# Kernel optimization log

Measured on AMD Instinct MI355X. Metric: run time of the kernel, lower is better.

Reference implementation:

```python
import jax, jax.numpy as jnp
import numpy as np

E = 1024      # embed_dim (== embed_dim_)
NH = 8        # num_heads
HD = E // NH  # head_dim
BS1 = 2048
BS2 = 2048
EPS = 1e-5


def _layernorm(x, g, b):
    m = jnp.mean(x, axis=-1, keepdims=True)
    v = jnp.mean(jnp.square(x - m), axis=-1, keepdims=True)
    return (x - m) * jax.lax.rsqrt(v + EPS) * g + b


def setup_inputs() -> dict:
    key = jax.random.key(0)
    ks = jax.random.split(key, 16)
    s = 1.0 / np.sqrt(E)
    s4 = 1.0 / np.sqrt(4 * E)
    inp = {
        "x1": jax.random.normal(ks[0], (BS1, E), jnp.float32),
        "x2": jax.random.normal(ks[1], (BS2, E), jnp.float32),
        "Wq": jax.random.uniform(ks[2], (E, E), jnp.float32, -s, s),
        "bq": jax.random.uniform(ks[3], (E,), jnp.float32, -s, s),
        "Wk": jax.random.uniform(ks[4], (E, E), jnp.float32, -s, s),
        "bk": jax.random.uniform(ks[5], (E,), jnp.float32, -s, s),
        "Wv": jax.random.uniform(ks[6], (E, E), jnp.float32, -s, s),
        "bv": jax.random.uniform(ks[7], (E,), jnp.float32, -s, s),
        "Wo": jax.random.uniform(ks[8], (E, E), jnp.float32, -s, s),
        "bo": jax.random.uniform(ks[9], (E,), jnp.float32, -s, s),
        "W1": jax.random.uniform(ks[10], (4 * E, E), jnp.float32, -s, s),
        "b1": jax.random.uniform(ks[11], (4 * E,), jnp.float32, -s, s),
        "W2": jax.random.uniform(ks[12], (E, 4 * E), jnp.float32, -s4, s4),
        "b2": jax.random.uniform(ks[13], (E,), jnp.float32, -s4, s4),
        "g1": jnp.ones((E,), jnp.float32),
        "be1": jnp.zeros((E,), jnp.float32),
        "g2": jnp.ones((E,), jnp.float32),
        "be2": jnp.zeros((E,), jnp.float32),
    }
    return inp


def reference(x1, x2, Wq, bq, Wk, bk, Wv, bv, Wo, bo, W1, b1, W2, b2, g1, be1, g2, be2):
    scale = HD ** -0.5
    # Projections; attention runs over the batch axis (n=bs1, m=bs2)
    q = (x1 @ Wq.T + bq).reshape(BS1, NH, HD)   # [n,h,d]
    k = (x2 @ Wk.T + bk).reshape(BS2, NH, HD)   # [m,h,d]
    v = (x2 @ Wv.T + bv).reshape(BS2, NH, HD)   # [m,h,d]
    scores = jnp.einsum('nhd,mhd->nmh', q, k) * scale  # [n,m,h]
    # NOTE: faithful to source: softmax over the HEADS axis (dim=-1)
    probs = jax.nn.softmax(scores, axis=-1)
    # dropout is identity in eval mode
    attn = jnp.einsum('nmh,mhd->nhd', probs, v).reshape(BS1, E)
    attn = attn @ Wo.T + bo
    h = _layernorm(x1 + attn, g1, be1)
    ffn = jax.nn.relu(h @ W1.T + b1) @ W2.T + b2
    return _layernorm(h + ffn, g2, be2)
```

## Files before the change

kernel.cpp:

```cpp
#include <hip/hip_runtime.h>

#define BS 2048
#define EMB 1024
#define NHEAD 8
#define HDIM 128

typedef unsigned short u16;
typedef __attribute__((ext_vector_type(8))) short bf16x8;
typedef __attribute__((ext_vector_type(4))) float f32x4;

__device__ __forceinline__ u16 f32_bf16(float f) {
  unsigned u = __float_as_uint(f);
  u += 0x7fffu + ((u >> 16) & 1u);
  return (u16)(u >> 16);
}
__device__ __forceinline__ float bf2f(u16 x) {
  return __uint_as_float((unsigned)x << 16);
}

__device__ __forceinline__ void gld_lds16(const void* g, void* l) {
  __builtin_amdgcn_global_load_lds(
      (const __attribute__((address_space(1))) void*)g,
      (__attribute__((address_space(3))) void*)l, 16, 0, 0);
}

struct CvtArgs { const float* src[8]; };
__global__ __launch_bounds__(256) void cvt_all(CvtArgs a, u16* __restrict__ dst) {
  long i = (long)blockIdx.x * 256 + threadIdx.x;
  int seg = (int)(i >> 18);
  const float* src; long b;
  if (seg < 2)       { src = a.src[0]; b = 0; }
  else if (seg < 4)  { src = a.src[1]; b = 2L << 18; }
  else if (seg == 4) { src = a.src[2]; b = 4L << 18; }
  else if (seg == 5) { src = a.src[3]; b = 5L << 18; }
  else if (seg == 6) { src = a.src[4]; b = 6L << 18; }
  else if (seg == 7) { src = a.src[5]; b = 7L << 18; }
  else if (seg < 12) { src = a.src[6]; b = 8L << 18; }
  else               { src = a.src[7]; b = 12L << 18; }
  float4 v = ((const float4*)src)[i - b];
  ushort4 o;
  o.x = f32_bf16(v.x); o.y = f32_bf16(v.y); o.z = f32_bf16(v.z); o.w = f32_bf16(v.w);
  ((ushort4*)dst)[i] = o;
}

__device__ __forceinline__ void gemm_core(
    const u16* __restrict__ A, const u16* __restrict__ B, void* __restrict__ Cp,
    const float* __restrict__ bias, int K, int lda, int ldb, int ldc,
    long cbase, int mode, int relu, int m0, int n0) {
  __shared__ __align__(16) u16 As[128 * 32];
  __shared__ __align__(16) u16 Bs[128 * 32];
  const int t = threadIdx.x;
  const int lane = t & 63, l15 = lane & 15, quad = lane >> 4;
  const int wv = t >> 6, wr = wv & 1, wc = wv >> 1;
  const int wbase = t & ~63;

  f32x4 acc[4][4];
#pragma unroll
  for (int r = 0; r < 4; ++r)
#pragma unroll
    for (int c = 0; c < 4; ++c) acc[r][c] = (f32x4){0.f, 0.f, 0.f, 0.f};

  for (int k0 = 0; k0 < K; k0 += 32) {
#pragma unroll
    for (int i = 0; i < 2; ++i) {
      int s = i * 256 + t;
      gld_lds16(A + (long)(m0 + (s >> 2)) * lda + k0 + (s & 3) * 8,
                As + (i * 256 + wbase) * 8);
    }
#pragma unroll
    for (int i = 0; i < 2; ++i) {
      int s = i * 256 + t;
      gld_lds16(B + (long)(n0 + (s >> 2)) * ldb + k0 + (s & 3) * 8,
                Bs + (i * 256 + wbase) * 8);
    }
    __syncthreads();
    bf16x8 fa[4], fb[4];
#pragma unroll
    for (int r = 0; r < 4; ++r)
      fa[r] = *(const bf16x8*)&As[(wr * 64 + r * 16 + l15) * 32 + quad * 8];
#pragma unroll
    for (int c = 0; c < 4; ++c)
      fb[c] = *(const bf16x8*)&Bs[(wc * 64 + c * 16 + l15) * 32 + quad * 8];
#pragma unroll
    for (int r = 0; r < 4; ++r)
#pragma unroll
      for (int c = 0; c < 4; ++c)
        acc[r][c] = __builtin_amdgcn_mfma_f32_16x16x32_bf16(fa[r], fb[c], acc[r][c], 0, 0, 0);
    __syncthreads();
  }

#pragma unroll
  for (int r = 0; r < 4; ++r)
#pragma unroll
    for (int c = 0; c < 4; ++c) {
      const int m = m0 + wr * 64 + r * 16 + quad * 4;
      const int n = n0 + wc * 64 + c * 16 + l15;
      const float bv = bias ? bias[n] : 0.f;
      f32x4 v = acc[r][c];
      if (mode == 2) {
        ushort4 o;
        o.x = f32_bf16(v[0] + bv);
        o.y = f32_bf16(v[1] + bv);
        o.z = f32_bf16(v[2] + bv);
        o.w = f32_bf16(v[3] + bv);
        *(ushort4*)((u16*)Cp + cbase + (long)n * ldc + m) = o;
      } else {
#pragma unroll
        for (int i = 0; i < 4; ++i) {
          float x = v[i] + bv;
          if (relu) x = fmaxf(x, 0.f);
          if (mode == 0)
            ((float*)Cp)[cbase + (long)(m + i) * ldc + n] = x;
          else
            ((u16*)Cp)[cbase + (long)(m + i) * ldc + n] = f32_bf16(x);
        }
      }
    }
}

__global__ __launch_bounds__(256) void gemm_bt_k(
    const u16* __restrict__ A, const u16* __restrict__ B, void* __restrict__ C,
    const float* __restrict__ bias, int K, int lda, int ldb, int ldc,
    long aOffZ, long bOffZ, long cOffZ, int mode, int relu) {
  gemm_core(A + (long)blockIdx.z * aOffZ, B + (long)blockIdx.z * bOffZ, C, bias,
            K, lda, ldb, ldc, (long)blockIdx.z * cOffZ, mode, relu,
            blockIdx.y * 128, blockIdx.x * 128);
}

__global__ __launch_bounds__(256) void qkv_kernel(
    const u16* __restrict__ x1b, const u16* __restrict__ x2b,
    const u16* __restrict__ Wqb, const u16* __restrict__ Wkb, const u16* __restrict__ Wvb,
    const float* __restrict__ bq, const float* __restrict__ bk, const float* __restrict__ bv,
    u16* __restrict__ Qb, u16* __restrict__ Kb, u16* __restrict__ Vt) {
  const int z = blockIdx.z;
  const u16* A = (z == 0) ? x1b : x2b;
  const u16* B = (z == 0) ? Wqb : (z == 1) ? Wkb : Wvb;
  void* C = (z == 0) ? (void*)Qb : (z == 1) ? (void*)Kb : (void*)Vt;
  const float* bias = (z == 0) ? bq : (z == 1) ? bk : bv;
  const int mode = (z == 2) ? 2 : 1;
  const int ldc = (z == 2) ? 2048 : 1024;
  gemm_core(A, B, C, bias, 1024, 1024, 1024, ldc, 0, mode, 0,
            blockIdx.y * 128, blockIdx.x * 128);
}

__global__ __launch_bounds__(512, 4) void attn_fused(
    const u16* __restrict__ Q, const u16* __restrict__ Km, const u16* __restrict__ Vt,
    u16* __restrict__ aP) {
  __shared__ __align__(16) u16 KQ[2 * 12288];
  __shared__ __align__(16) u16 Ps[8 * 32 * 64];
  const int t = threadIdx.x;
  const int lane = t & 63, l15 = lane & 15, quad = lane >> 4;
  const int w = t >> 6;
  const int mw = w & 3, nh = w >> 2;
  const int lin = blockIdx.x + (int)gridDim.x * blockIdx.y;
  const int g = lin & 7, u = lin >> 3;
  const int my = (g >> 1) * 2 + (u & 1);
  const int nx = (g & 1) * 32 + (u >> 1);
  const int n0 = nx * 32;
  const int mz = my * 256;
  u16* part = aP + (long)my * BS * 1024;

  auto stage = [&](int snum, int bsel) {
    const int sh = (snum & 7) * 128;
    const int smb = mz + (snum >> 3) * 64;
#pragma unroll
    for (int i = 0; i < 3; ++i) {
      int G = i * 512 + t;
      int r = G >> 4, gg = G & 15;
      const u16* src;
      if (i < 2) src = Km + (long)(smb + r) * 1024 + sh + ((gg ^ (r & 7)) << 3);
      else       src = Q + (long)(n0 + r - 64) * 1024 + sh + ((gg ^ (r & 7)) << 3);
      gld_lds16(src, KQ + bsel * 12288 + G * 8);
    }
  };

  f32x4 accp[2][8];
#pragma unroll
  for (int r = 0; r < 2; ++r)
#pragma unroll
    for (int c = 0; c < 8; ++c) accp[r][c] = (f32x4){0.f, 0.f, 0.f, 0.f};

  int b = 0;
  stage(0, 0);

  const int m = mw * 16 + l15;
  const int nq = nh * 16 + l15;
  const int sw3 = (l15 & 7) << 3;
  const int sw4 = (l15 & 7) << 4;

  for (int it = 0; it < 4; ++it) {
    const int mb = mz + it * 64;
    f32x4 accs[8];
#pragma unroll
    for (int h = 0; h < 8; ++h) accs[h] = (f32x4){0.f, 0.f, 0.f, 0.f};

#pragma unroll
    for (int h = 0; h < 8; ++h) {
      __syncthreads();
      int ns = it * 8 + h + 1;
      if (ns < 32) stage(ns, b ^ 1);
      const u16* kb = KQ + b * 12288;
      const u16* qb = kb + 64 * 128;
#pragma unroll
      for (int kk = 0; kk < 4; ++kk) {
        int ko = (kk * 32 + quad * 8) ^ sw3;
        bf16x8 fa = *(const bf16x8*)&kb[m * 128 + ko];
        bf16x8 fb = *(const bf16x8*)&qb[nq * 128 + ko];
        accs[h] = __builtin_amdgcn_mfma_f32_16x16x32_bf16(fa, fb, accs[h], 0, 0, 0);
      }
      b ^= 1;
    }

    const float scale = 0.08838834764831845f;
#pragma unroll
    for (int i = 0; i < 4; ++i) {
      float mx = accs[0][i];
#pragma unroll
      for (int h = 1; h < 8; ++h) mx = fmaxf(mx, accs[h][i]);
      float sum = 0.f;
#pragma unroll
      for (int h = 0; h < 8; ++h) {
        float e = __expf((accs[h][i] - mx) * scale);
        accs[h][i] = e;
        sum += e;
      }
      float inv = 1.f / sum;
#pragma unroll
      for (int h = 0; h < 8; ++h) accs[h][i] *= inv;
    }
#pragma unroll
    for (int h = 0; h < 8; ++h) {
      ushort4 o;
      o.x = f32_bf16(accs[h][0]);
      o.y = f32_bf16(accs[h][1]);
      o.z = f32_bf16(accs[h][2]);
      o.w = f32_bf16(accs[h][3]);
      *(ushort4*)((char*)Ps + h * 4096 + nq * 128 + ((mw * 32 + quad * 8) ^ sw4)) = o;
    }
    __syncthreads();
#pragma unroll
    for (int mq = 0; mq < 2; ++mq) {
      bf16x8 vf[8];
#pragma unroll
      for (int c = 0; c < 8; ++c)
        vf[c] = *(const bf16x8*)&Vt[(long)(w * 128 + c * 16 + l15) * 2048 +
                                    mb + mq * 32 + quad * 8];
      bf16x8 pa[2];
#pragma unroll
      for (int r = 0; r < 2; ++r)
        pa[r] = *(const bf16x8*)((const char*)Ps + w * 4096 + (r * 16 + l15) * 128 +
                                 ((mq * 64 + quad * 16) ^ sw4));
#pragma unroll
      for (int c = 0; c < 8; ++c)
#pragma unroll
        for (int r = 0; r < 2; ++r)
          accp[r][c] = __builtin_amdgcn_mfma_f32_16x16x32_bf16(pa[r], vf[c], accp[r][c], 0, 0, 0);
    }
  }
#pragma unroll
  for (int r = 0; r < 2; ++r)
#pragma unroll
    for (int c = 0; c < 8; ++c)
#pragma unroll
      for (int i = 0; i < 4; ++i)
        part[(long)(n0 + r * 16 + quad * 4 + i) * 1024 + w * 128 + c * 16 + l15] =
            f32_bf16(accp[r][c][i]);
}

__global__ __launch_bounds__(256) void reduce8p_bf16(
    const u16* __restrict__ base, u16* __restrict__ out) {
  long i = (long)blockIdx.x * 256 + threadIdx.x;
  const long stride = (long)BS * 1024 / 4;
  float sx = 0.f, sy = 0.f, sz = 0.f, sw = 0.f;
#pragma unroll
  for (int k = 0; k < 8; ++k) {
    ushort4 a = ((const ushort4*)base)[i + k * stride];
    sx += bf2f(a.x); sy += bf2f(a.y); sz += bf2f(a.z); sw += bf2f(a.w);
  }
  ushort4 o;
  o.x = f32_bf16(sx); o.y = f32_bf16(sy); o.z = f32_bf16(sz); o.w = f32_bf16(sw);
  ((ushort4*)out)[i] = o;
}

__global__ __launch_bounds__(256) void ln_residual_p4(
    const float* __restrict__ x,
    const u16* __restrict__ p0, const u16* __restrict__ p1,
    const u16* __restrict__ p2, const u16* __restrict__ p3,
    const float* __restrict__ colb, const float* __restrict__ g, const float* __restrict__ b,
    float* __restrict__ out32, u16* __restrict__ out16) {
  const int row = blockIdx.x, t = threadIdx.x;
  const long base = (long)row * EMB;
  float4 v = ((const float4*)(x + base))[t];
  ushort4 a0 = ((const ushort4*)(p0 + base))[t];
  ushort4 a1 = ((const ushort4*)(p1 + base))[t];
  ushort4 a2 = ((const ushort4*)(p2 + base))[t];
  ushort4 a3 = ((const ushort4*)(p3 + base))[t];
  float4 cb = ((const float4*)colb)[t];
  v.x += bf2f(a0.x) + bf2f(a1.x) + bf2f(a2.x) + bf2f(a3.x) + cb.x;
  v.y += bf2f(a0.y) + bf2f(a1.y) + bf2f(a2.y) + bf2f(a3.y) + cb.y;
  v.z += bf2f(a0.z) + bf2f(a1.z) + bf2f(a2.z) + bf2f(a3.z) + cb.z;
  v.w += bf2f(a0.w) + bf2f(a1.w) + bf2f(a2.w) + bf2f(a3.w) + cb.w;
  float s = v.x + v.y + v.z + v.w;
  float q = v.x * v.x + v.y * v.y + v.z * v.z + v.w * v.w;
#pragma unroll
  for (int off = 32; off > 0; off >>= 1) {
    s += __shfl_xor(s, off);
    q += __shfl_xor(q, off);
  }
  __shared__ float red[8];
  const int wv = t >> 6, lane = t & 63;
  if (lane == 0) { red[wv] = s; red[4 + wv] = q; }
  __syncthreads();
  s = red[0] + red[1] + red[2] + red[3];
  q = red[4] + red[5] + red[6] + red[7];
  const float mean = s * (1.f / EMB);
  const float var = q * (1.f / EMB) - mean * mean;
  const float rstd = rsqrtf(var + 1e-5f);
  float4 gg = ((const float4*)g)[t];
  float4 bb = ((const float4*)b)[t];
  float4 o;
  o.x = (v.x - mean) * rstd * gg.x + bb.x;
  o.y = (v.y - mean) * rstd * gg.y + bb.y;
  o.z = (v.z - mean) * rstd * gg.z + bb.z;
  o.w = (v.w - mean) * rstd * gg.w + bb.w;
  ((float4*)(out32 + base))[t] = o;
  if (out16) {
    ushort4 ho;
    ho.x = f32_bf16(o.x); ho.y = f32_bf16(o.y); ho.z = f32_bf16(o.z); ho.w = f32_bf16(o.w);
    ((ushort4*)(out16 + base))[t] = ho;
  }
}

extern "C" void kernel_launch(void* const* d_in, const int* in_sizes, int n_in,
                              void* d_out, int out_size, void* d_ws, size_t ws_size,
                              hipStream_t stream) {
  const float* x1 = (const float*)d_in[0];
  const float* x2 = (const float*)d_in[1];
  const float* Wq = (const float*)d_in[2];
  const float* bq = (const float*)d_in[3];
  const float* Wk = (const float*)d_in[4];
  const float* bk = (const float*)d_in[5];
  const float* Wv = (const float*)d_in[6];
  const float* bv = (const float*)d_in[7];
  const float* Wo = (const float*)d_in[8];
  const float* bo = (const float*)d_in[9];
  const float* W1 = (const float*)d_in[10];
  const float* b1 = (const float*)d_in[11];
  const float* W2 = (const float*)d_in[12];
  const float* b2 = (const float*)d_in[13];
  const float* g1 = (const float*)d_in[14];
  const float* be1 = (const float*)d_in[15];
  const float* g2 = (const float*)d_in[16];
  const float* be2 = (const float*)d_in[17];

  char* ws = (char*)d_ws;
  const size_t MB = 1ull << 20;
  u16* x1b = (u16*)(ws + 0 * MB);
  u16* x2b = (u16*)(ws + 4 * MB);
  u16* Wqb = (u16*)(ws + 8 * MB);
  u16* Wkb = (u16*)(ws + 10 * MB);
  u16* Wvb = (u16*)(ws + 12 * MB);
  u16* Wob = (u16*)(ws + 14 * MB);
  u16* W1b = (u16*)(ws + 16 * MB);
  u16* W2b = (u16*)(ws + 24 * MB);
  u16* Qb  = (u16*)(ws + 32 * MB);
  u16* Kb  = (u16*)(ws + 36 * MB);
  u16* Vtb = (u16*)(ws + 40 * MB);
  u16* attnb = (u16*)(ws + 44 * MB);
  u16* aP = (u16*)(ws + 48 * MB);
  u16* woP[4] = {(u16*)(ws + 48 * MB), (u16*)(ws + 52 * MB),
                 (u16*)(ws + 56 * MB), (u16*)(ws + 60 * MB)};
  float* h32  = (float*)(ws + 64 * MB);
  u16*  h16   = (u16*)(ws + 72 * MB);
  u16*  ffn1b = (u16*)(ws + 76 * MB);
  u16* f2P[4] = {(u16*)(ws + 92 * MB), (u16*)(ws + 96 * MB),
                 (u16*)(ws + 100 * MB), (u16*)(ws + 104 * MB)};

  CvtArgs ca;
  ca.src[0] = x1; ca.src[1] = x2; ca.src[2] = Wq; ca.src[3] = Wk;
  ca.src[4] = Wv; ca.src[5] = Wo; ca.src[6] = W1; ca.src[7] = W2;
  cvt_all<<<16384, 256, 0, stream>>>(ca, (u16*)ws);

  qkv_kernel<<<dim3(8, 16, 3), 256, 0, stream>>>(x1b, x2b, Wqb, Wkb, Wvb, bq, bk, bv, Qb, Kb, Vtb);

  attn_fused<<<dim3(64, 8), 512, 0, stream>>>(Qb, Kb, Vtb, aP);

  reduce8p_bf16<<<2048, 256, 0, stream>>>(aP, attnb);

  gemm_bt_k<<<dim3(8, 16, 4), 256, 0, stream>>>(attnb, Wob, woP[0], nullptr,
                                                256, 1024, 1024, 1024,
                                                256, 256, (long)BS * 1024, 1, 0);

  ln_residual_p4<<<2048, 256, 0, stream>>>(x1, woP[0], woP[1], woP[2], woP[3],
                                           bo, g1, be1, h32, h16);

  gemm_bt_k<<<dim3(32, 16, 1), 256, 0, stream>>>(h16, W1b, ffn1b, b1,
                                                 1024, 1024, 1024, 4096,
                                                 0, 0, 0, 1, 1);

  gemm_bt_k<<<dim3(8, 16, 4), 256, 0, stream>>>(ffn1b, W2b, f2P[0], nullptr,
                                                1024, 4096, 4096, 1024,
                                                1024, 1024, (long)BS * 1024, 1, 0);

  ln_residual_p4<<<2048, 256, 0, stream>>>(h32, f2P[0], f2P[1], f2P[2], f2P[3],
                                           b2, g2, be2, (float*)d_out, nullptr);
}
```

Measured before the change: 358.4 us.

## Halve attention m-split to 4 and use 4-stage LDS pipeline with manual waitcnt

The attention kernel now splits the key axis into 4 chunks of 512 instead of 8 of 256. This halves the partial-output writes and turns the reduction into a 4-way sum. The K/Q staging moves from a 2-buffer ring to a 4-buffer ring with a prefetch distance of 3. Syncthreads are replaced by explicit vmcnt/lgkmcnt waits plus raw barriers, so async global-to-LDS loads stay in flight longer. The cost is double the LDS (occupancy bound lowered to 2 blocks/SM), half the blocks in the grid, and reliance on hand-counted wait values being correct.

```diff
diff --git a/kernel.cpp b/kernel.cpp
--- a/kernel.cpp
+++ b/kernel.cpp
@@ -143,10 +143,10 @@
             blockIdx.y * 128, blockIdx.x * 128);
 }
 
-__global__ __launch_bounds__(512, 4) void attn_fused(
+__global__ __launch_bounds__(512, 2) void attn_fused(
     const u16* __restrict__ Q, const u16* __restrict__ Km, const u16* __restrict__ Vt,
-    u16* __restrict__ aP) {
-  __shared__ __align__(16) u16 KQ[2 * 12288];
+    u16* __restrict__ p0, u16* __restrict__ p1, u16* __restrict__ p2, u16* __restrict__ p3) {
+  __shared__ __align__(16) u16 KQ[4 * 12288];
   __shared__ __align__(16) u16 Ps[8 * 32 * 64];
   const int t = threadIdx.x;
   const int lane = t & 63, l15 = lane & 15, quad = lane >> 4;
@@ -154,11 +154,11 @@
   const int mw = w & 3, nh = w >> 2;
   const int lin = blockIdx.x + (int)gridDim.x * blockIdx.y;
   const int g = lin & 7, u = lin >> 3;
-  const int my = (g >> 1) * 2 + (u & 1);
-  const int nx = (g & 1) * 32 + (u >> 1);
+  const int my = g >> 1;
+  const int nx = (g & 1) * 32 + u;
   const int n0 = nx * 32;
-  const int mz = my * 256;
-  u16* part = aP + (long)my * BS * 1024;
+  const int mz = my * 512;
+  u16* part = (my == 0) ? p0 : (my == 1) ? p1 : (my == 2) ? p2 : p3;
 
   auto stage = [&](int snum, int bsel) {
     const int sh = (snum & 7) * 128;
@@ -180,15 +180,16 @@
 #pragma unroll
     for (int c = 0; c < 8; ++c) accp[r][c] = (f32x4){0.f, 0.f, 0.f, 0.f};
 
-  int b = 0;
   stage(0, 0);
+  stage(1, 1);
+  stage(2, 2);
 
   const int m = mw * 16 + l15;
   const int nq = nh * 16 + l15;
   const int sw3 = (l15 & 7) << 3;
   const int sw4 = (l15 & 7) << 4;
 
-  for (int it = 0; it < 4; ++it) {
+  for (int it = 0; it < 8; ++it) {
     const int mb = mz + it * 64;
     f32x4 accs[8];
 #pragma unroll
@@ -196,10 +197,14 @@
 
 #pragma unroll
     for (int h = 0; h < 8; ++h) {
-      __syncthreads();
-      int ns = it * 8 + h + 1;
-      if (ns < 32) stage(ns, b ^ 1);
-      const u16* kb = KQ + b * 12288;
+      const int s = it * 8 + h;
+      if (s <= 61)      asm volatile("s_waitcnt vmcnt(6)" ::: "memory");
+      else if (s == 62) asm volatile("s_waitcnt vmcnt(3)" ::: "memory");
+      else              asm volatile("s_waitcnt vmcnt(0)" ::: "memory");
+      __builtin_amdgcn_s_barrier();
+      __builtin_amdgcn_sched_barrier(0);
+      if (s + 3 < 64) stage(s + 3, (h + 3) & 3);
+      const u16* kb = KQ + (h & 3) * 12288;
       const u16* qb = kb + 64 * 128;
 #pragma unroll
       for (int kk = 0; kk < 4; ++kk) {
@@ -208,7 +213,6 @@
         bf16x8 fb = *(const bf16x8*)&qb[nq * 128 + ko];
         accs[h] = __builtin_amdgcn_mfma_f32_16x16x32_bf16(fa, fb, accs[h], 0, 0, 0);
       }
-      b ^= 1;
     }
 
     const float scale = 0.08838834764831845f;
@@ -237,7 +241,9 @@
       o.w = f32_bf16(accs[h][3]);
       *(ushort4*)((char*)Ps + h * 4096 + nq * 128 + ((mw * 32 + quad * 8) ^ sw4)) = o;
     }
-    __syncthreads();
+    asm volatile("s_waitcnt lgkmcnt(0)" ::: "memory");
+    __builtin_amdgcn_s_barrier();
+    __builtin_amdgcn_sched_barrier(0);
 #pragma unroll
     for (int mq = 0; mq < 2; ++mq) {
       bf16x8 vf[8];
@@ -267,18 +273,19 @@
             f32_bf16(accp[r][c][i]);
 }
 
-__global__ __launch_bounds__(256) void reduce8p_bf16(
-    const u16* __restrict__ base, u16* __restrict__ out) {
+__global__ __launch_bounds__(256) void reduce4p_bf16(
+    const u16* __restrict__ p0, const u16* __restrict__ p1,
+    const u16* __restrict__ p2, const u16* __restrict__ p3, u16* __restrict__ out) {
   long i = (long)blockIdx.x * 256 + threadIdx.x;
-  const long stride = (long)BS * 1024 / 4;
-  float sx = 0.f, sy = 0.f, sz = 0.f, sw = 0.f;
-#pragma unroll
-  for (int k = 0; k < 8; ++k) {
-    ushort4 a = ((const ushort4*)base)[i + k * stride];
-    sx += bf2f(a.x); sy += bf2f(a.y); sz += bf2f(a.z); sw += bf2f(a.w);
-  }
+  ushort4 a = ((const ushort4*)p0)[i];
+  ushort4 b = ((const ushort4*)p1)[i];
+  ushort4 c = ((const ushort4*)p2)[i];
+  ushort4 d = ((const ushort4*)p3)[i];
   ushort4 o;
-  o.x = f32_bf16(sx); o.y = f32_bf16(sy); o.z = f32_bf16(sz); o.w = f32_bf16(sw);
+  o.x = f32_bf16(bf2f(a.x) + bf2f(b.x) + bf2f(c.x) + bf2f(d.x));
+  o.y = f32_bf16(bf2f(a.y) + bf2f(b.y) + bf2f(c.y) + bf2f(d.y));
+  o.z = f32_bf16(bf2f(a.z) + bf2f(b.z) + bf2f(c.z) + bf2f(d.z));
+  o.w = f32_bf16(bf2f(a.w) + bf2f(b.w) + bf2f(c.w) + bf2f(d.w));
   ((ushort4*)out)[i] = o;
 }
 
@@ -367,7 +374,8 @@
   u16* Kb  = (u16*)(ws + 36 * MB);
   u16* Vtb = (u16*)(ws + 40 * MB);
   u16* attnb = (u16*)(ws + 44 * MB);
-  u16* aP = (u16*)(ws + 48 * MB);
+  u16* aP[4] = {(u16*)(ws + 48 * MB), (u16*)(ws + 52 * MB),
+                (u16*)(ws + 56 * MB), (u16*)(ws + 60 * MB)};
   u16* woP[4] = {(u16*)(ws + 48 * MB), (u16*)(ws + 52 * MB),
                  (u16*)(ws + 56 * MB), (u16*)(ws + 60 * MB)};
   float* h32  = (float*)(ws + 64 * MB);
@@ -383,9 +391,9 @@
 
   qkv_kernel<<<dim3(8, 16, 3), 256, 0, stream>>>(x1b, x2b, Wqb, Wkb, Wvb, bq, bk, bv, Qb, Kb, Vtb);
 
-  attn_fused<<<dim3(64, 8), 512, 0, stream>>>(Qb, Kb, Vtb, aP);
-
-  reduce8p_bf16<<<2048, 256, 0, stream>>>(aP, attnb);
+  attn_fused<<<dim3(64, 4), 512, 0, stream>>>(Qb, Kb, Vtb, aP[0], aP[1], aP[2], aP[3]);
+
+  reduce4p_bf16<<<2048, 256, 0, stream>>>(aP[0], aP[1], aP[2], aP[3], attnb);
 
   gemm_bt_k<<<dim3(8, 16, 4), 256, 0, stream>>>(attnb, Wob, woP[0], nullptr,
                                                 256, 1024, 1024, 1024,
```

Measured after the change: 335.8 us. -6.3%, faster.
